# Performance work log

Hardware: AMD Instinct MI355X
Metric: run time of the kernel (lower is better)

## Reference

```python
import jax, jax.numpy as jnp
import numpy as np

N_NODES = 50000


def gcn_conv(x, src, dst, W, b):
    # PyG GCNConv: h = D^-1/2 (A+I) D^-1/2 (x W) + b, aggregation at dst.
    n = x.shape[0]
    deg = jax.ops.segment_sum(jnp.ones_like(dst, dtype=x.dtype), dst, num_segments=n)
    dinv = jnp.where(deg > 0, jax.lax.rsqrt(deg), 0.0)
    norm = dinv[src] * dinv[dst]                      # [E]
    h = x @ W                                         # [N, out]
    msg = h[src] * norm[:, None]                      # [E, out] gather
    out = jax.ops.segment_sum(msg, dst, num_segments=n)  # scatter-add
    return out + b


def setup_inputs() -> dict:
    key = jax.random.key(0)
    k1, k2, k3, k4 = jax.random.split(key, 4)
    in_dim, hid, out_dim = 128, 256, 128
    x = jax.random.normal(k1, (N_NODES, in_dim), dtype=jnp.float32)
    edge_index = jax.random.randint(k2, (2, 800000), 0, N_NODES, dtype=jnp.int64)
    s1 = 1.0 / np.sqrt(in_dim)
    s2 = 1.0 / np.sqrt(hid)
    W1 = jax.random.uniform(k3, (in_dim, hid), jnp.float32, -s1, s1)
    b1 = jnp.zeros((hid,), jnp.float32)
    W2 = jax.random.uniform(k4, (hid, out_dim), jnp.float32, -s2, s2)
    b2 = jnp.zeros((out_dim,), jnp.float32)
    return {"x": x, "edge_index": edge_index, "W1": W1, "b1": b1, "W2": W2, "b2": b2}


def reference(x, edge_index, W1, b1, W2, b2):
    n = x.shape[0]
    loops = jnp.arange(n, dtype=edge_index.dtype)
    src = jnp.concatenate([edge_index[0], loops])  # add self-loops
    dst = jnp.concatenate([edge_index[1], loops])
    h = jax.nn.relu(gcn_conv(x, src, dst, W1, b1))
    # dropout in eval mode -> identity
    return gcn_conv(h, src, dst, W2, b2)
```

## Files before the change

kernel.cpp:

```cpp
#include <hip/hip_runtime.h>
#include <hip/hip_bf16.h>


typedef __bf16 bf16x8v __attribute__((ext_vector_type(8)));
typedef short  s16x8   __attribute__((ext_vector_type(8)));
typedef float  f32x4   __attribute__((ext_vector_type(4)));

#define IN_DIM 128
#define HID    256
#define OUTD   128
#define BKT_SHIFT 7
#define BKT_NODES 128
#define MAXB 512
#define CAP  8192

__device__ __forceinline__ float2 bf2f(__hip_bfloat162 v) {
    return make_float2(__bfloat162float(v.x), __bfloat162float(v.y));
}
__device__ __forceinline__ __hip_bfloat162 f2bf(float a, float b) {
    __hip_bfloat162 r; r.x = __float2bfloat16(a); r.y = __float2bfloat16(b); return r;
}

__global__ void k_detect(const void* W2raw, const void* eiraw, int* flags) {
    if (threadIdx.x != 0 || blockIdx.x != 0) return;
    const unsigned short* u = (const unsigned short*)W2raw;
    int f32 = 0;
    for (int i = 0; i < 64; ++i) {
        unsigned e = (u[i] >> 7) & 0xFF;
        if (e >= 0x7F) f32 = 1;
    }
    const unsigned* ip = (const unsigned*)eiraw;
    unsigned orodd = 0;
    for (int i = 0; i < 64; ++i) orodd |= ip[2 * i + 1];
    flags[0] = f32;
    flags[1] = (orodd == 0) ? 1 : 0;
}


__device__ __forceinline__ short ldw(const void* raw, int idx, int f32) {
    if (f32) {
        __hip_bfloat16 h = __float2bfloat16(((const float*)raw)[idx]);
        return *(short*)&h;
    }
    return ((const short*)raw)[idx];
}

template <int K, int NN>
__device__ __forceinline__ void swz_one(const void* Wraw, int f32,
                                        short* __restrict__ Bsw, int tid) {
    constexpr int KC = K / 32;
    constexpr int NT = NN / 16;
    if (tid >= NT * KC * 64) return;
    int lane = tid & 63;
    int kc   = (tid >> 6) % KC;
    int nt   = tid / (64 * KC);
    int n  = nt * 16 + (lane & 15);
    int kb = kc * 32 + (lane >> 4) * 8;
    s16x8 v;
#pragma unroll
    for (int j = 0; j < 8; ++j) v[j] = ldw(Wraw, (kb + j) * NN + n, f32);
    ((s16x8*)Bsw)[tid] = v;
}

__global__ __launch_bounds__(256) void k_prep_w(
        const void* W1raw, const void* b1raw, const void* W2raw, const void* b2raw,
        const int* __restrict__ flags, short* __restrict__ Bsw1, short* __restrict__ Bsw2,
        __hip_bfloat16* __restrict__ b1c, __hip_bfloat16* __restrict__ b2c) {
    int f32 = flags[0];
    int blk = blockIdx.x, t = threadIdx.x;
    if (blk < 16) {
        swz_one<IN_DIM, HID>(W1raw, f32, Bsw1, blk * 256 + t);
    } else if (blk < 32) {
        swz_one<HID, OUTD>(W2raw, f32, Bsw2, (blk - 16) * 256 + t);
    } else {
        short s1 = ldw(b1raw, t, f32);
        b1c[t] = *(__hip_bfloat16*)&s1;
        if (t < OUTD) {
            short s2 = ldw(b2raw, t, f32);
            b2c[t] = *(__hip_bfloat16*)&s2;
        }
    }
}


__global__ __launch_bounds__(256) void k_edges(
        const void* __restrict__ ei_, int E, int N, int NB,
        const int* __restrict__ flags, int* __restrict__ bcnt,
        unsigned* __restrict__ ppack) {
    __shared__ int lhist[MAXB], lbase[MAXB];
    int i64 = flags[1];
    const long long* p64 = (const long long*)ei_;
    const int*       p32 = (const int*)ei_;
    int per = (E + gridDim.x - 1) / gridDim.x;
    int e0 = blockIdx.x * per, e1 = min(e0 + per, E);
    for (int i = threadIdx.x; i < NB; i += 256) lhist[i] = 0;
    __syncthreads();
    for (int e = e0 + threadIdx.x; e < e1; e += 256) {
        int d = i64 ? (int)p64[E + e] : p32[E + e];
        if ((unsigned)d >= (unsigned)N) d = 0;
        atomicAdd(&lhist[((unsigned)d) >> BKT_SHIFT], 1);
    }
    __syncthreads();
    for (int i = threadIdx.x; i < NB; i += 256) {
        int c = lhist[i];
        lbase[i] = c ? atomicAdd(&bcnt[i], c) : 0;
        lhist[i] = 0;
    }
    __syncthreads();
    for (int e = e0 + threadIdx.x; e < e1; e += 256) {
        int d = i64 ? (int)p64[E + e] : p32[E + e];
        int s = i64 ? (int)p64[e]     : p32[e];
        if ((unsigned)d >= (unsigned)N) d = 0;
        if ((unsigned)s >= (unsigned)N) s = 0;
        int b = ((unsigned)d) >> BKT_SHIFT;
        int pos = lbase[b] + atomicAdd(&lhist[b], 1);
        if (pos < CAP)
            ppack[(size_t)b * CAP + pos] = ((unsigned)(d & (BKT_NODES - 1)) << 25) | (unsigned)s;
    }
}

__global__ __launch_bounds__(512) void k_bscan(int* __restrict__ bcnt, int NB,
                                               int* __restrict__ boff,
                                               int* __restrict__ offsets, float* __restrict__ dinv,
                                               int N, int Npad) {
    __shared__ int s[MAXB];
    int t = threadIdx.x;
    int c = (t < NB) ? min(bcnt[t], CAP) : 0;
    if (t < NB) bcnt[t] = c;
    s[t] = c; __syncthreads();
    for (int off = 1; off < MAXB; off <<= 1) {
        int u = (t >= off) ? s[t - off] : 0;
        __syncthreads();
        s[t] += u;
        __syncthreads();
    }
    if (t < NB) boff[t] = s[t] - c;
    if (t == 0) { int tot = s[MAXB - 1]; boff[NB] = tot; offsets[N] = tot; }
    if (t < Npad - N) dinv[N + t] = 0.f;
}

__global__ __launch_bounds__(256) void k_bsort(const int* __restrict__ boff,
                                               const int* __restrict__ bcnt,
                                               const unsigned* __restrict__ ppack,
                                               int* __restrict__ csr, int* __restrict__ offsets,
                                               float* __restrict__ dinv, int N) {
    __shared__ int h[BKT_NODES], base[BKT_NODES], s[BKT_NODES];
    int b = blockIdx.x;
    int ebase = boff[b], cnt = bcnt[b];
    const unsigned* pp = ppack + (size_t)b * CAP;
    int t = threadIdx.x;
    if (t < BKT_NODES) h[t] = 0;
    __syncthreads();
    for (int e = t; e < cnt; e += 256) atomicAdd(&h[pp[e] >> 25], 1);
    __syncthreads();
    int v = (t < BKT_NODES) ? h[t] : 0;
    if (t < BKT_NODES) s[t] = v;
    __syncthreads();
    for (int off = 1; off < BKT_NODES; off <<= 1) {
        int u = (t < BKT_NODES && t >= off) ? s[t - off] : 0;
        __syncthreads();
        if (t < BKT_NODES) s[t] += u;
        __syncthreads();
    }
    if (t < BKT_NODES) {
        int excl = s[t] - v;
        base[t] = excl;
        int node = b * BKT_NODES + t;
        if (node < N) {
            offsets[node] = ebase + excl;
            dinv[node] = rsqrtf((float)(v + 1));
        }
        h[t] = 0;
    }
    __syncthreads();
    for (int e = t; e < cnt; e += 256) {
        unsigned pk = pp[e];
        int ld = pk >> 25;
        int pos = ebase + base[ld] + atomicAdd(&h[ld], 1);
        csr[pos] = (int)(pk & 0x1FFFFFFu);
    }
}


__global__ __launch_bounds__(256) void k_prescale_x(
        const void* __restrict__ xraw, const float* __restrict__ dinv,
        const int* __restrict__ flags, __hip_bfloat162* __restrict__ xs2,
        int N, int Npad) {
    int gid = blockIdx.x * 256 + threadIdx.x;
    int v = gid >> 6, lane = gid & 63;
    if (v >= Npad) return;
    __hip_bfloat162 val;
    if (v < N) {
        float dv = dinv[v];
        float2 t = flags[0] ? ((const float2*)xraw)[(size_t)v * 64 + lane]
                            : bf2f(((const __hip_bfloat162*)xraw)[(size_t)v * 64 + lane]);
        val = f2bf(dv * t.x, dv * t.y);
    } else val = f2bf(0.f, 0.f);
    xs2[(size_t)v * 64 + lane] = val;
}


__global__ __launch_bounds__(256) void k_agg1(
        const __hip_bfloat162* __restrict__ xs2, const int* __restrict__ offsets,
        const int* __restrict__ csr, const float* __restrict__ dinv,
        __hip_bfloat162* __restrict__ a2, int N, int Npad, int nwaves) {
    int gw   = blockIdx.x * 4 + (threadIdx.x >> 6);
    int lane = threadIdx.x & 63;
    for (int v = gw; v < Npad; v += nwaves) {
        if (v >= N) { a2[(size_t)v * 64 + lane] = f2bf(0.f, 0.f); continue; }
        float2 s0v = bf2f(xs2[(size_t)v * 64 + lane]);
        float ax = s0v.x, ay = s0v.y;
        int e = offsets[v], o1 = offsets[v + 1];
        for (; e + 3 < o1; e += 4) {
            int s0 = csr[e], s1 = csr[e + 1], s2 = csr[e + 2], s3 = csr[e + 3];
            float2 t0 = bf2f(xs2[(size_t)s0 * 64 + lane]);
            float2 t1 = bf2f(xs2[(size_t)s1 * 64 + lane]);
            float2 t2 = bf2f(xs2[(size_t)s2 * 64 + lane]);
            float2 t3 = bf2f(xs2[(size_t)s3 * 64 + lane]);
            ax += (t0.x + t1.x) + (t2.x + t3.x);
            ay += (t0.y + t1.y) + (t2.y + t3.y);
        }
        for (; e < o1; ++e) {
            int s = csr[e];
            float2 t = bf2f(xs2[(size_t)s * 64 + lane]);
            ax += t.x; ay += t.y;
        }
        float dv = dinv[v];
        a2[(size_t)v * 64 + lane] = f2bf(dv * ax, dv * ay);
    }
}


template <int K, int NN, bool RELU_BIAS>
__global__ __launch_bounds__(256) void k_gemm(
        const __hip_bfloat16* __restrict__ A, const __hip_bfloat16* __restrict__ Bsw,
        const __hip_bfloat16* __restrict__ bias, const float* __restrict__ dinv,
        __hip_bfloat16* __restrict__ C) {
    constexpr int KC = K / 32;
    constexpr int NT = NN / 16;
    int wave = threadIdx.x >> 6, lane = threadIdx.x & 63;
    int quad = lane >> 4, l16 = lane & 15;
    int m0 = blockIdx.x * 128 + wave * 32;

    bf16x8v a[2][KC];
#pragma unroll
    for (int st = 0; st < 2; ++st)
#pragma unroll
        for (int kc = 0; kc < KC; ++kc)
            a[st][kc] = *reinterpret_cast<const bf16x8v*>(
                A + (size_t)(m0 + st * 16 + l16) * K + kc * 32 + quad * 8);

    const bf16x8v* B8 = reinterpret_cast<const bf16x8v*>(Bsw);
    int rb0 = m0 + quad * 4, rb1 = m0 + 16 + quad * 4;
    float sc0[4], sc1[4];
    if (!RELU_BIAS) {
#pragma unroll
        for (int r = 0; r < 4; ++r) { sc0[r] = dinv[rb0 + r]; sc1[r] = dinv[rb1 + r]; }
    }

    for (int nt = 0; nt < NT; ++nt) {
        f32x4 acc0 = {0.f, 0.f, 0.f, 0.f}, acc1 = {0.f, 0.f, 0.f, 0.f};
#pragma unroll
        for (int kc = 0; kc < KC; ++kc) {
            bf16x8v bfrag = B8[(nt * KC + kc) * 64 + lane];
            acc0 = __builtin_amdgcn_mfma_f32_16x16x32_bf16(a[0][kc], bfrag, acc0, 0, 0, 0);
            acc1 = __builtin_amdgcn_mfma_f32_16x16x32_bf16(a[1][kc], bfrag, acc1, 0, 0, 0);
        }
        int col = nt * 16 + l16;
        if (RELU_BIAS) {
            float bv = __bfloat162float(bias[col]);
#pragma unroll
            for (int r = 0; r < 4; ++r) {
                float v0 = acc0[r] + bv; v0 = v0 > 0.f ? v0 : 0.f;
                float v1 = acc1[r] + bv; v1 = v1 > 0.f ? v1 : 0.f;
                C[(size_t)(rb0 + r) * NN + col] = __float2bfloat16(v0);
                C[(size_t)(rb1 + r) * NN + col] = __float2bfloat16(v1);
            }
        } else {
#pragma unroll
            for (int r = 0; r < 4; ++r) {
                C[(size_t)(rb0 + r) * NN + col] = __float2bfloat16(acc0[r] * sc0[r]);
                C[(size_t)(rb1 + r) * NN + col] = __float2bfloat16(acc1[r] * sc1[r]);
            }
        }
    }
}


__global__ __launch_bounds__(256) void k_agg2(
        const __hip_bfloat162* __restrict__ h22, const int* __restrict__ offsets,
        const int* __restrict__ csr, const float* __restrict__ dinv,
        const __hip_bfloat16* __restrict__ b2c, const int* __restrict__ flags,
        void* __restrict__ outraw, int N, int nwaves) {
    int gw   = blockIdx.x * 4 + (threadIdx.x >> 6);
    int lane = threadIdx.x & 63;
    int f32  = flags[0];
    float2 bb = bf2f(((const __hip_bfloat162*)b2c)[lane]);
    for (int v = gw; v < N; v += nwaves) {
        float2 a = bf2f(h22[(size_t)v * 64 + lane]);
        float ax = a.x, ay = a.y;
        int e = offsets[v], o1 = offsets[v + 1];
        for (; e + 3 < o1; e += 4) {
            int s0 = csr[e], s1 = csr[e + 1], s2 = csr[e + 2], s3 = csr[e + 3];
            float2 t0 = bf2f(h22[(size_t)s0 * 64 + lane]);
            float2 t1 = bf2f(h22[(size_t)s1 * 64 + lane]);
            float2 t2 = bf2f(h22[(size_t)s2 * 64 + lane]);
            float2 t3 = bf2f(h22[(size_t)s3 * 64 + lane]);
            ax += (t0.x + t1.x) + (t2.x + t3.x);
            ay += (t0.y + t1.y) + (t2.y + t3.y);
        }
        for (; e < o1; ++e) {
            int s = csr[e];
            float2 t = bf2f(h22[(size_t)s * 64 + lane]);
            ax += t.x; ay += t.y;
        }
        float dv = dinv[v];
        float ox = dv * ax + bb.x, oy = dv * ay + bb.y;
        if (f32) ((float2*)outraw)[(size_t)v * 64 + lane] = make_float2(ox, oy);
        else     ((__hip_bfloat162*)outraw)[(size_t)v * 64 + lane] = f2bf(ox, oy);
    }
}


extern "C" void kernel_launch(void* const* d_in, const int* in_sizes, int n_in,
                              void* d_out, int out_size, void* d_ws, size_t ws_size,
                              hipStream_t stream) {
    const void* x  = d_in[0];
    const void* ei = d_in[1];
    const void* W1 = d_in[2];
    const void* b1 = d_in[3];
    const void* W2 = d_in[4];
    const void* b2 = d_in[5];

    const int N = in_sizes[0] / IN_DIM;
    const int E = in_sizes[1] / 2;
    const int Npad = ((N + 127) / 128) * 128;
    const int NB = (N + BKT_NODES - 1) / BKT_NODES;

    char* w = (char*)d_ws;
    auto alloc = [&](size_t bytes) -> void* {
        void* p = (void*)w;
        w += (bytes + 255) / 256 * 256;
        return p;
    };
    int*   flags   = (int*)alloc(256);
    int*   bcnt    = (int*)alloc((size_t)MAXB * 4);
    int*   boff    = (int*)alloc((size_t)(MAXB + 1) * 4);
    int*   offsets = (int*)alloc((size_t)(N + 1) * 4);
    float* dinv    = (float*)alloc((size_t)Npad * 4);
    unsigned* ppack = (unsigned*)alloc((size_t)NB * CAP * 4);
    int*   csr     = (int*)alloc((size_t)E * 4);
    short* Bsw1 = (short*)alloc((size_t)IN_DIM * HID * 2);
    short* Bsw2 = (short*)alloc((size_t)HID * OUTD * 2);
    __hip_bfloat16* b1c = (__hip_bfloat16*)alloc((size_t)HID * 2);
    __hip_bfloat16* b2c = (__hip_bfloat16*)alloc((size_t)OUTD * 2);
    __hip_bfloat16* xs  = (__hip_bfloat16*)alloc((size_t)Npad * IN_DIM * 2);
    __hip_bfloat16* a1  = (__hip_bfloat16*)alloc((size_t)Npad * IN_DIM * 2);
    __hip_bfloat16* h1  = (__hip_bfloat16*)alloc((size_t)Npad * HID * 2);
    __hip_bfloat16* h2s = xs;

    k_detect<<<1, 64, 0, stream>>>(W2, ei, flags);
    hipMemsetAsync(bcnt, 0, (size_t)MAXB * 4, stream);

    k_prep_w<<<33, 256, 0, stream>>>(W1, b1, W2, b2, flags, Bsw1, Bsw2, b1c, b2c);

    k_edges<<<64, 256, 0, stream>>>(ei, E, N, NB, flags, bcnt, ppack);
    k_bscan<<<1, MAXB, 0, stream>>>(bcnt, NB, boff, offsets, dinv, N, Npad);
    k_bsort<<<NB, 256, 0, stream>>>(boff, bcnt, ppack, csr, offsets, dinv, N);

    k_prescale_x<<<(Npad * 64 + 255) / 256, 256, 0, stream>>>(x, dinv, flags,
                                                              (__hip_bfloat162*)xs, N, Npad);

    const int aggBlocks = 2048, nwaves = aggBlocks * 4;
    k_agg1<<<aggBlocks, 256, 0, stream>>>((const __hip_bfloat162*)xs, offsets, csr, dinv,
                                          (__hip_bfloat162*)a1, N, Npad, nwaves);

    k_gemm<IN_DIM, HID, true><<<Npad / 128, 256, 0, stream>>>(
        a1, (const __hip_bfloat16*)Bsw1, b1c, nullptr, h1);
    k_gemm<HID, OUTD, false><<<Npad / 128, 256, 0, stream>>>(
        h1, (const __hip_bfloat16*)Bsw2, nullptr, dinv, h2s);

    k_agg2<<<aggBlocks, 256, 0, stream>>>((const __hip_bfloat162*)h2s, offsets, csr, dinv,
                                          b2c, flags, d_out, N, nwaves);
}
```

Baseline: 252.9 us.

## Fuse x prescale into bucket sort, privatize edge histograms per wave, widen edge grid

Folds the x row-scaling by dinv into the bucket-sort kernel, so each bucket block scales its own 128 nodes using dinv kept in shared memory, and the separate prescale kernel launch is removed. The edge-bucketing kernel now keeps one shared histogram per wave, which cuts LDS atomic contention, and runs on 512 blocks instead of 64 for more parallelism. The cost is more global atomics on the bucket counters. The type-detection kernel now uses a wave ballot instead of a serial single-thread loop.

Result: faster. 233.6 us (-7.6%).

```diff
diff --git a/kernel.cpp b/kernel.cpp
--- a/kernel.cpp
+++ b/kernel.cpp
@@ -13,6 +13,7 @@
 #define BKT_NODES 128
 #define MAXB 512
 #define CAP  8192
+#define EBLK 512
 
 __device__ __forceinline__ float2 bf2f(__hip_bfloat162 v) {
     return make_float2(__bfloat162float(v.x), __bfloat162float(v.y));
@@ -22,18 +23,16 @@
 }
 
 __global__ void k_detect(const void* W2raw, const void* eiraw, int* flags) {
-    if (threadIdx.x != 0 || blockIdx.x != 0) return;
+    int lane = threadIdx.x;
     const unsigned short* u = (const unsigned short*)W2raw;
-    int f32 = 0;
-    for (int i = 0; i < 64; ++i) {
-        unsigned e = (u[i] >> 7) & 0xFF;
-        if (e >= 0x7F) f32 = 1;
-    }
+    unsigned e = (u[lane] >> 7) & 0xFF;
+    unsigned long long m1 = __ballot(e >= 0x7F);
     const unsigned* ip = (const unsigned*)eiraw;
-    unsigned orodd = 0;
-    for (int i = 0; i < 64; ++i) orodd |= ip[2 * i + 1];
-    flags[0] = f32;
-    flags[1] = (orodd == 0) ? 1 : 0;
+    unsigned long long m2 = __ballot(ip[2 * lane + 1] != 0);
+    if (lane == 0) {
+        flags[0] = (m1 != 0) ? 1 : 0;
+        flags[1] = (m2 == 0) ? 1 : 0;
+    }
 }
 
 
@@ -87,24 +86,33 @@
         const void* __restrict__ ei_, int E, int N, int NB,
         const int* __restrict__ flags, int* __restrict__ bcnt,
         unsigned* __restrict__ ppack) {
-    __shared__ int lhist[MAXB], lbase[MAXB];
+    __shared__ int lhist[4][MAXB];
+    __shared__ int lbase[4][MAXB];
+    int wv = threadIdx.x >> 6;
     int i64 = flags[1];
     const long long* p64 = (const long long*)ei_;
     const int*       p32 = (const int*)ei_;
     int per = (E + gridDim.x - 1) / gridDim.x;
     int e0 = blockIdx.x * per, e1 = min(e0 + per, E);
-    for (int i = threadIdx.x; i < NB; i += 256) lhist[i] = 0;
+    for (int i = threadIdx.x; i < NB; i += 256) {
+        lhist[0][i] = 0; lhist[1][i] = 0; lhist[2][i] = 0; lhist[3][i] = 0;
+    }
     __syncthreads();
     for (int e = e0 + threadIdx.x; e < e1; e += 256) {
         int d = i64 ? (int)p64[E + e] : p32[E + e];
         if ((unsigned)d >= (unsigned)N) d = 0;
-        atomicAdd(&lhist[((unsigned)d) >> BKT_SHIFT], 1);
+        atomicAdd(&lhist[wv][((unsigned)d) >> BKT_SHIFT], 1);
     }
     __syncthreads();
     for (int i = threadIdx.x; i < NB; i += 256) {
-        int c = lhist[i];
-        lbase[i] = c ? atomicAdd(&bcnt[i], c) : 0;
-        lhist[i] = 0;
+        int c0 = lhist[0][i], c1 = lhist[1][i], c2 = lhist[2][i], c3 = lhist[3][i];
+        int tot = c0 + c1 + c2 + c3;
+        int g = tot ? atomicAdd(&bcnt[i], tot) : 0;
+        lbase[0][i] = g;
+        lbase[1][i] = g + c0;
+        lbase[2][i] = g + c0 + c1;
+        lbase[3][i] = g + c0 + c1 + c2;
+        lhist[0][i] = 0; lhist[1][i] = 0; lhist[2][i] = 0; lhist[3][i] = 0;
     }
     __syncthreads();
     for (int e = e0 + threadIdx.x; e < e1; e += 256) {
@@ -113,7 +121,7 @@
         if ((unsigned)d >= (unsigned)N) d = 0;
         if ((unsigned)s >= (unsigned)N) s = 0;
         int b = ((unsigned)d) >> BKT_SHIFT;
-        int pos = lbase[b] + atomicAdd(&lhist[b], 1);
+        int pos = lbase[wv][b] + atomicAdd(&lhist[wv][b], 1);
         if (pos < CAP)
             ppack[(size_t)b * CAP + pos] = ((unsigned)(d & (BKT_NODES - 1)) << 25) | (unsigned)s;
     }
@@ -143,8 +151,12 @@
                                                const int* __restrict__ bcnt,
                                                const unsigned* __restrict__ ppack,
                                                int* __restrict__ csr, int* __restrict__ offsets,
-                                               float* __restrict__ dinv, int N) {
+                                               float* __restrict__ dinv, int N,
+                                               const void* __restrict__ xraw,
+                                               const int* __restrict__ flags,
+                                               __hip_bfloat16* __restrict__ xs) {
     __shared__ int h[BKT_NODES], base[BKT_NODES], s[BKT_NODES];
+    __shared__ float sdv[BKT_NODES];
     int b = blockIdx.x;
     int ebase = boff[b], cnt = bcnt[b];
     const unsigned* pp = ppack + (size_t)b * CAP;
@@ -166,10 +178,13 @@
         int excl = s[t] - v;
         base[t] = excl;
         int node = b * BKT_NODES + t;
+        float dv = 0.f;
         if (node < N) {
+            dv = rsqrtf((float)(v + 1));
             offsets[node] = ebase + excl;
-            dinv[node] = rsqrtf((float)(v + 1));
-        }
+            dinv[node] = dv;
+        }
+        sdv[t] = dv;
         h[t] = 0;
     }
     __syncthreads();
@@ -179,24 +194,44 @@
         int pos = ebase + base[ld] + atomicAdd(&h[ld], 1);
         csr[pos] = (int)(pk & 0x1FFFFFFu);
     }
-}
-
-
-__global__ __launch_bounds__(256) void k_prescale_x(
-        const void* __restrict__ xraw, const float* __restrict__ dinv,
-        const int* __restrict__ flags, __hip_bfloat162* __restrict__ xs2,
-        int N, int Npad) {
-    int gid = blockIdx.x * 256 + threadIdx.x;
-    int v = gid >> 6, lane = gid & 63;
-    if (v >= Npad) return;
-    __hip_bfloat162 val;
-    if (v < N) {
-        float dv = dinv[v];
-        float2 t = flags[0] ? ((const float2*)xraw)[(size_t)v * 64 + lane]
-                            : bf2f(((const __hip_bfloat162*)xraw)[(size_t)v * 64 + lane]);
-        val = f2bf(dv * t.x, dv * t.y);
-    } else val = f2bf(0.f, 0.f);
-    xs2[(size_t)v * 64 + lane] = val;
+    int f32 = flags[0];
+    if (!f32) {
+        const s16x8* xg = (const s16x8*)xraw;
+        s16x8* xo = (s16x8*)xs;
+        for (int u = t; u < BKT_NODES * 16; u += 256) {
+            int row = u >> 4;
+            int node = b * BKT_NODES + row;
+            float dv = sdv[row];
+            s16x8 val = {0, 0, 0, 0, 0, 0, 0, 0};
+            if (node < N) {
+                s16x8 xin = xg[(size_t)node * 16 + (u & 15)];
+                __hip_bfloat162* xp = (__hip_bfloat162*)&xin;
+                __hip_bfloat162* vp = (__hip_bfloat162*)&val;
+#pragma unroll
+                for (int j = 0; j < 4; ++j) {
+                    float2 f = bf2f(xp[j]);
+                    vp[j] = f2bf(dv * f.x, dv * f.y);
+                }
+            }
+            xo[(size_t)node * 16 + (u & 15)] = val;
+        }
+    } else {
+        const float4* xg = (const float4*)xraw;
+        __hip_bfloat162* xo = (__hip_bfloat162*)xs;
+        for (int u = t; u < BKT_NODES * 32; u += 256) {
+            int row = u >> 5;
+            int node = b * BKT_NODES + row;
+            float dv = sdv[row];
+            __hip_bfloat162 v0 = f2bf(0.f, 0.f), v1 = v0;
+            if (node < N) {
+                float4 xin = xg[(size_t)node * 32 + (u & 31)];
+                v0 = f2bf(dv * xin.x, dv * xin.y);
+                v1 = f2bf(dv * xin.z, dv * xin.w);
+            }
+            xo[(size_t)node * 64 + (u & 31) * 2]     = v0;
+            xo[(size_t)node * 64 + (u & 31) * 2 + 1] = v1;
+        }
+    }
 }
 
 
@@ -364,12 +399,10 @@
 
     k_prep_w<<<33, 256, 0, stream>>>(W1, b1, W2, b2, flags, Bsw1, Bsw2, b1c, b2c);
 
-    k_edges<<<64, 256, 0, stream>>>(ei, E, N, NB, flags, bcnt, ppack);
+    k_edges<<<EBLK, 256, 0, stream>>>(ei, E, N, NB, flags, bcnt, ppack);
     k_bscan<<<1, MAXB, 0, stream>>>(bcnt, NB, boff, offsets, dinv, N, Npad);
-    k_bsort<<<NB, 256, 0, stream>>>(boff, bcnt, ppack, csr, offsets, dinv, N);
-
-    k_prescale_x<<<(Npad * 64 + 255) / 256, 256, 0, stream>>>(x, dinv, flags,
-                                                              (__hip_bfloat162*)xs, N, Npad);
+    k_bsort<<<NB, 256, 0, stream>>>(boff, bcnt, ppack, csr, offsets, dinv, N,
+                                    x, flags, xs);
 
     const int aggBlocks = 2048, nwaves = aggBlocks * 4;
     k_agg1<<<aggBlocks, 256, 0, stream>>>((const __hip_bfloat162*)xs, offsets, csr, dinv,
```
